# Kernel tuning notes

Hardware: AMD Instinct MI355X
Metric: run time of the kernel (lower is better)

The kernel has to match this reference:

```python
import jax, jax.numpy as jnp
import numpy as np

ANCHORS = np.array([[10.0, 13.0, 8.0], [16.0, 30.0, 12.0], [33.0, 23.0, 20.0]], dtype=np.float32)
NUM_ANCHORS = 3
NUM_CLASSES = 5
BBOX_ATTRS = 5 + NUM_CLASSES
IMG_SIZE = (256, 256, 256)  # (W, H, D)


def setup_inputs() -> dict:
    key = jax.random.key(0)
    B, D, H, W = 4, 64, 64, 64
    x = jax.random.normal(key, (B, NUM_ANCHORS * BBOX_ATTRS, D, H, W), dtype=jnp.float32)
    return {"input": x}


def reference(input):
    B = input.shape[0]
    D, H, W = input.shape[2], input.shape[3], input.shape[4]
    stride_w = IMG_SIZE[0] / W
    stride_h = IMG_SIZE[1] / H
    stride_d = IMG_SIZE[2] / D

    # [B, A, attrs, D, H, W] -> [B, A, D, H, W, attrs]
    pred = input.reshape(B, NUM_ANCHORS, BBOX_ATTRS, D, H, W).transpose(0, 1, 3, 4, 5, 2)

    x = jax.nn.sigmoid(pred[..., 0])
    y = jax.nn.sigmoid(pred[..., 1])
    z = jax.nn.sigmoid(pred[..., 2])
    l = pred[..., 3]
    conf = jax.nn.sigmoid(pred[..., 4])
    pred_cls = jax.nn.sigmoid(pred[..., 5:])

    # Broadcasted grids (replaces the O(B*A*D*H*W) python loops)
    grid_x = jnp.arange(W, dtype=jnp.float32)                      # broadcasts over last axis
    grid_y = jnp.arange(H, dtype=jnp.float32)[:, None]             # over H
    grid_z = jnp.arange(D, dtype=jnp.float32)[:, None, None]       # over D

    # Only anchor width (scaled) is used for the box length
    anchor_w = jnp.asarray(ANCHORS[:, 0] / stride_w)[None, :, None, None, None]  # [1,A,1,1,1]

    sw = jnp.float32(stride_w)
    sh = jnp.float32(stride_h)
    sd = jnp.float32(stride_d)

    bx = (x + grid_x) * sw
    by = (y + grid_y) * sh
    bz = (z + grid_z) * sd
    bl = jnp.exp(l) * anchor_w * sw

    boxes = jnp.stack([bx, by, bz, bl], axis=-1)                   # [B,A,D,H,W,4]
    n = NUM_ANCHORS * D * H * W
    out = jnp.concatenate([
        boxes.reshape(B, n, 4),
        conf.reshape(B, n, 1),
        pred_cls.reshape(B, n, NUM_CLASSES),
    ], axis=-1)
    return out
```

## Files before the change

kernel.cpp:

```cpp
#include <hip/hip_runtime.h>
#include <math.h>


constexpr int A_NUM  = 3;
constexpr int ATTRS  = 10;
constexpr int DD = 64, HH = 64, WW = 64;
constexpr int SPATIAL = DD * HH * WW;
constexpr int BLOCK = 256;
constexpr int ROWS_PER_THREAD = 4;
constexpr int CHUNK_ROWS = BLOCK * ROWS_PER_THREAD;
constexpr int CHUNK_VEC4 = CHUNK_ROWS * ATTRS / 4;

__device__ __forceinline__ float sigmoidf_fast(float x) {
    return 1.0f / (1.0f + __expf(-x));
}

__global__ __launch_bounds__(256) void decode_box_kernel(const float* __restrict__ in,
                                                         float* __restrict__ out) {
    __shared__ float4 tile[CHUNK_VEC4];

    int tid = threadIdx.x;
    int t   = blockIdx.x * BLOCK + tid;

    int idx = t << 2;
    int s   = idx & (SPATIAL - 1);
    int ba  = idx >> 18;
    int a   = ba % A_NUM;
    int w   = s & (WW - 1);
    int h   = (s >> 6) & (HH - 1);
    int d   = s >> 12;

    const float* base = in + (size_t)ba * ATTRS * SPATIAL + s;

    float p[ATTRS][4];
#pragma unroll
    for (int k = 0; k < ATTRS; ++k) {
        float4 v = *reinterpret_cast<const float4*>(base + (size_t)k * SPATIAL);
        p[k][0] = v.x; p[k][1] = v.y; p[k][2] = v.z; p[k][3] = v.w;
    }

    float aw = (a == 0) ? 10.0f : (a == 1 ? 16.0f : 33.0f);
    float fh = (float)h * 4.0f;
    float fd = (float)d * 4.0f;

    float o[4 * ATTRS];
#pragma unroll
    for (int j = 0; j < 4; ++j) {
        float* oj = o + j * ATTRS;
        oj[0] = sigmoidf_fast(p[0][j]) * 4.0f + (float)(w + j) * 4.0f;
        oj[1] = sigmoidf_fast(p[1][j]) * 4.0f + fh;
        oj[2] = sigmoidf_fast(p[2][j]) * 4.0f + fd;
        oj[3] = __expf(p[3][j]) * aw;
        oj[4] = sigmoidf_fast(p[4][j]);
#pragma unroll
        for (int c = 0; c < 5; ++c)
            oj[5 + c] = sigmoidf_fast(p[5 + c][j]);
    }

#pragma unroll
    for (int i = 0; i < ATTRS; ++i)
        tile[tid * ATTRS + i] = make_float4(o[4 * i], o[4 * i + 1], o[4 * i + 2], o[4 * i + 3]);

    __syncthreads();

    float4* o4 = reinterpret_cast<float4*>(out) + (size_t)blockIdx.x * CHUNK_VEC4;
#pragma unroll
    for (int i = 0; i < ATTRS; ++i)
        o4[i * BLOCK + tid] = tile[i * BLOCK + tid];
}

extern "C" void kernel_launch(void* const* d_in, const int* in_sizes, int n_in,
                              void* d_out, int out_size, void* d_ws, size_t ws_size,
                              hipStream_t stream) {
    const float* in = (const float*)d_in[0];
    float* out = (float*)d_out;

    int total  = in_sizes[0] / ATTRS;
    int blocks = total / CHUNK_ROWS;

    decode_box_kernel<<<blocks, BLOCK, 0, stream>>>(in, out);
}
```

Measured before the change: 42.32 us.

## Process eight rows per thread with swizzled per-wave LDS staging and nontemporal stores

Each thread now handles eight spatial positions, issuing two vector loads per attribute, and a scheduling barrier groups all loads before the math. The output transpose goes through a smaller LDS tile one wave at a time over four passes, with an XOR swizzle to cut bank conflicts, and the final writes use nontemporal stores. The goal is fewer blocks, more memory-level parallelism per thread and less cache pollution from the write-once output. In exchange there is higher register pressure, which may lower occupancy, and four serialized sync passes per block.

```diff
diff --git a/kernel.cpp b/kernel.cpp
--- a/kernel.cpp
+++ b/kernel.cpp
@@ -1,15 +1,18 @@
 #include <hip/hip_runtime.h>
 #include <math.h>
 
+
+typedef float v4f __attribute__((ext_vector_type(4)));
 
 constexpr int A_NUM  = 3;
 constexpr int ATTRS  = 10;
 constexpr int DD = 64, HH = 64, WW = 64;
 constexpr int SPATIAL = DD * HH * WW;
 constexpr int BLOCK = 256;
-constexpr int ROWS_PER_THREAD = 4;
+constexpr int ROWS_PER_THREAD = 8;
 constexpr int CHUNK_ROWS = BLOCK * ROWS_PER_THREAD;
 constexpr int CHUNK_VEC4 = CHUNK_ROWS * ATTRS / 4;
+constexpr int PASS_VEC4  = CHUNK_VEC4 / 4;
 
 __device__ __forceinline__ float sigmoidf_fast(float x) {
     return 1.0f / (1.0f + __expf(-x));
@@ -17,12 +20,13 @@
 
 __global__ __launch_bounds__(256) void decode_box_kernel(const float* __restrict__ in,
                                                          float* __restrict__ out) {
-    __shared__ float4 tile[CHUNK_VEC4];
+    __shared__ v4f tile[PASS_VEC4];
 
     int tid = threadIdx.x;
-    int t   = blockIdx.x * BLOCK + tid;
+    int wid = tid >> 6;
+    int lt  = tid & 63;
 
-    int idx = t << 2;
+    int idx = (blockIdx.x * BLOCK + tid) << 3;
     int s   = idx & (SPATIAL - 1);
     int ba  = idx >> 18;
     int a   = ba % A_NUM;
@@ -32,41 +36,67 @@
 
     const float* base = in + (size_t)ba * ATTRS * SPATIAL + s;
 
-    float p[ATTRS][4];
+    v4f L[20];
 #pragma unroll
     for (int k = 0; k < ATTRS; ++k) {
-        float4 v = *reinterpret_cast<const float4*>(base + (size_t)k * SPATIAL);
-        p[k][0] = v.x; p[k][1] = v.y; p[k][2] = v.z; p[k][3] = v.w;
+        L[2 * k]     = *reinterpret_cast<const v4f*>(base + (size_t)k * SPATIAL);
+        L[2 * k + 1] = *reinterpret_cast<const v4f*>(base + (size_t)k * SPATIAL + 4);
     }
+    __builtin_amdgcn_sched_barrier(0);
 
     float aw = (a == 0) ? 10.0f : (a == 1 ? 16.0f : 33.0f);
+    float fw = (float)w * 4.0f;
     float fh = (float)h * 4.0f;
     float fd = (float)d * 4.0f;
 
-    float o[4 * ATTRS];
 #pragma unroll
-    for (int j = 0; j < 4; ++j) {
-        float* oj = o + j * ATTRS;
-        oj[0] = sigmoidf_fast(p[0][j]) * 4.0f + (float)(w + j) * 4.0f;
-        oj[1] = sigmoidf_fast(p[1][j]) * 4.0f + fh;
-        oj[2] = sigmoidf_fast(p[2][j]) * 4.0f + fd;
-        oj[3] = __expf(p[3][j]) * aw;
-        oj[4] = sigmoidf_fast(p[4][j]);
+    for (int k = 0; k < ATTRS; ++k) {
 #pragma unroll
-        for (int c = 0; c < 5; ++c)
-            oj[5 + c] = sigmoidf_fast(p[5 + c][j]);
+        for (int half = 0; half < 2; ++half) {
+#pragma unroll
+            for (int c = 0; c < 4; ++c) {
+                int j = half * 4 + c;
+                float x = L[2 * k + half][c];
+                float r;
+                if      (k == 0) r = sigmoidf_fast(x) * 4.0f + fw + (float)j * 4.0f;
+                else if (k == 1) r = sigmoidf_fast(x) * 4.0f + fh;
+                else if (k == 2) r = sigmoidf_fast(x) * 4.0f + fd;
+                else if (k == 3) r = __expf(x) * aw;
+                else             r = sigmoidf_fast(x);
+                L[2 * k + half][c] = r;
+            }
+        }
     }
 
+    v4f* o4 = reinterpret_cast<v4f*>(out) + (size_t)blockIdx.x * CHUNK_VEC4;
+
 #pragma unroll
-    for (int i = 0; i < ATTRS; ++i)
-        tile[tid * ATTRS + i] = make_float4(o[4 * i], o[4 * i + 1], o[4 * i + 2], o[4 * i + 3]);
-
-    __syncthreads();
-
-    float4* o4 = reinterpret_cast<float4*>(out) + (size_t)blockIdx.x * CHUNK_VEC4;
+    for (int p = 0; p < 4; ++p) {
+        if (wid == p) {
 #pragma unroll
-    for (int i = 0; i < ATTRS; ++i)
-        o4[i * BLOCK + tid] = tile[i * BLOCK + tid];
+            for (int i = 0; i < 20; ++i) {
+                v4f v;
+#pragma unroll
+                for (int c = 0; c < 4; ++c) {
+                    int g = 4 * i + c;
+                    int j = g / ATTRS;
+                    int k = g % ATTRS;
+                    v[c] = L[2 * k + (j >> 2)][j & 3];
+                }
+                int jj = lt * 20 + i;
+                tile[jj ^ (lt & 7)] = v;
+            }
+        }
+        __syncthreads();
+#pragma unroll
+        for (int i = 0; i < PASS_VEC4 / BLOCK; ++i) {
+            int j = i * BLOCK + tid;
+            unsigned q = (unsigned)j / 20u;
+            v4f v = tile[j ^ (int)(q & 7u)];
+            __builtin_nontemporal_store(v, &o4[p * PASS_VEC4 + j]);
+        }
+        if (p < 3) __syncthreads();
+    }
 }
 
 extern "C" void kernel_launch(void* const* d_in, const int* in_sizes, int n_in,
```

New measurement: 43.14 us. Within noise of the previous version (+1.9%).
